# Kernel tuning notes

Hardware: AMD Instinct MI355X
Metric: run time of the kernel (lower is better)

## Reference

```python
import jax, jax.numpy as jnp
import numpy as np

N, F, R, E = 10000, 128, 20, 640000

def _linear_params(key, fan_in, fan_out):
    k1, k2 = jax.random.split(key)
    bound = 1.0 / np.sqrt(fan_in)
    W = jax.random.uniform(k1, (fan_in, fan_out), jnp.float32, -bound, bound)
    b = jax.random.uniform(k2, (fan_out,), jnp.float32, -bound, bound)
    return W, b

def _mlp(x, W1, b1, W2, b2):
    # Linear -> SiLU -> Linear on last axis
    return jax.nn.silu(x @ W1 + b1) @ W2 + b2


def setup_inputs() -> dict:
    key = jax.random.key(0)
    ks = jax.random.split(key, 12)
    s = jax.random.normal(ks[0], (N, F), jnp.float32)
    v = jax.random.normal(ks[1], (N, 3, F), jnp.float32)
    edge_index = jax.random.randint(ks[2], (2, E), 0, N, jnp.int32)
    rbf = jax.random.normal(ks[3], (E, R), jnp.float32)
    ms_w1, ms_b1 = _linear_params(ks[4], F + R, F)
    ms_w2, ms_b2 = _linear_params(ks[5], F, F)
    mv_w1, mv_b1 = _linear_params(ks[6], F + R, F)
    mv_w2, mv_b2 = _linear_params(ks[7], F, F)
    us_w1, us_b1 = _linear_params(ks[8], 2 * F, F)
    us_w2, us_b2 = _linear_params(ks[9], F, F)
    uv_w1, uv_b1 = _linear_params(ks[10], 2 * F, F)
    uv_w2, uv_b2 = _linear_params(ks[11], F, F)
    return dict(s=s, v=v, edge_index=edge_index, rbf=rbf,
                ms_w1=ms_w1, ms_b1=ms_b1, ms_w2=ms_w2, ms_b2=ms_b2,
                mv_w1=mv_w1, mv_b1=mv_b1, mv_w2=mv_w2, mv_b2=mv_b2,
                us_w1=us_w1, us_b1=us_b1, us_w2=us_w2, us_b2=us_b2,
                uv_w1=uv_w1, uv_b1=uv_b1, uv_w2=uv_w2, uv_b2=uv_b2)


def reference(s, v, edge_index, rbf,
              ms_w1, ms_b1, ms_w2, ms_b2,
              mv_w1, mv_b1, mv_w2, mv_b2,
              us_w1, us_b1, us_w2, us_b2,
              uv_w1, uv_b1, uv_w2, uv_b2):
    row, col = edge_index[0], edge_index[1]
    n_nodes = s.shape[0]
    s_row = s[row]                                  # [E, F]
    v_diff = v[row] - v[col]                        # [E, 3, F]
    s_msg = jnp.concatenate([s_row, rbf], axis=-1)  # [E, F+R]
    # per-edge vector message input: broadcast scalar features over the 3 axis
    v_msg = jnp.concatenate([
        jnp.broadcast_to(s_row[:, None, :], (s_row.shape[0], 3, s.shape[1])),
        jnp.broadcast_to(rbf[:, None, :], (rbf.shape[0], 3, rbf.shape[1])),
    ], axis=-1)                                     # [E, 3, F+R]
    ds = _mlp(s_msg, ms_w1, ms_b1, ms_w2, ms_b2)    # [E, F]
    dv = _mlp(v_msg, mv_w1, mv_b1, mv_w2, mv_b2)    # [E, 3, F]
    # normalize v_diff per (edge, feature) over the 3-vector axis
    v_norm = jnp.linalg.norm(v_diff, axis=1, keepdims=True)  # [E, 1, F]
    dv = dv * (v_diff / (v_norm + 1e-08))
    ds_agg = jax.ops.segment_sum(ds, col, num_segments=n_nodes)  # [N, F]
    dv_agg = jax.ops.segment_sum(dv, col, num_segments=n_nodes)  # [N, 3, F]
    s_out = s + _mlp(jnp.concatenate([s, ds_agg], axis=-1), us_w1, us_b1, us_w2, us_b2)
    v_out = v + _mlp(jnp.concatenate([v, dv_agg], axis=-1), uv_w1, uv_b1, uv_w2, uv_b2)
    return (s_out, v_out)
```

## Files before the change

### kernel.cpp

```cpp
#include <hip/hip_runtime.h>

#define FDIM 128
#define NEDGE 640000
#define NNODE 10000
#define K1PAD 160
#define HSTR 136

typedef __attribute__((ext_vector_type(8))) short short8;
typedef __attribute__((ext_vector_type(4))) float f32x4;
typedef __attribute__((ext_vector_type(4))) unsigned short ushort4_t;

static __device__ __forceinline__ unsigned short f2bf(float f){
  unsigned int u = __builtin_bit_cast(unsigned int, f);
  u += 0x7fffu + ((u >> 16) & 1u);
  return (unsigned short)(u >> 16);
}
static __device__ __forceinline__ short8 pack8(const float* x){
  short8 r;
#pragma unroll
  for (int i = 0; i < 8; ++i) r[i] = (short)f2bf(x[i]);
  return r;
}
static __device__ __forceinline__ short8 cvt8(float4 a, float4 b){
  float x[8] = {a.x, a.y, a.z, a.w, b.x, b.y, b.z, b.w};
  return pack8(x);
}
static __device__ __forceinline__ f32x4 mfma16(short8 a, short8 b, f32x4 c){
  return __builtin_amdgcn_mfma_f32_16x16x32_bf16(a, b, c, 0, 0, 0);
}
static __device__ __forceinline__ float silu(float p){
  return p * (1.f / (1.f + __expf(-p)));
}

__global__ __launch_bounds__(256) void prep_wt(
    const float* __restrict__ ms_w1, const float* __restrict__ mv_w1,
    const float* __restrict__ ms_w2, const float* __restrict__ mv_w2,
    const float* __restrict__ us_w1, const float* __restrict__ uv_w1,
    const float* __restrict__ us_w2, const float* __restrict__ uv_w2,
    unsigned short* __restrict__ wbuf)
{
  int i = blockIdx.x * 256 + threadIdx.x;
  if (i >= 172032) return;
  float val;
  if (i < 40960) {
    int t = (i < 20480) ? i : i - 20480;
    const float* src = (i < 20480) ? ms_w1 : mv_w1;
    int j = t / 160, k = t - j * 160;
    val = (k < 148) ? src[k * 128 + j] : 0.f;
  } else if (i < 73728) {
    int t = i - 40960;
    const float* src = (t < 16384) ? ms_w2 : mv_w2;
    t &= 16383;
    int j = t >> 7, k = t & 127;
    val = src[k * 128 + j];
  } else if (i < 139264) {
    int t = i - 73728;
    const float* src = (t < 32768) ? us_w1 : uv_w1;
    t &= 32767;
    int j = t >> 8, k = t & 255;
    val = src[k * 128 + j];
  } else {
    int t = i - 139264;
    const float* src = (t < 16384) ? us_w2 : uv_w2;
    t &= 16383;
    int j = t >> 7, k = t & 127;
    val = src[k * 128 + j];
  }
  wbuf[i] = f2bf(val);
}

__global__ __launch_bounds__(256) void prep_misc(
    const float* __restrict__ s, unsigned short* __restrict__ s_bf,
    float* __restrict__ zero_base)
{
  int i = blockIdx.x * 256 + threadIdx.x;
  if (i < 320000) {
    float4 p = *reinterpret_cast<const float4*>(s + i * 4);
    ushort4_t o;
    o[0] = f2bf(p.x); o[1] = f2bf(p.y); o[2] = f2bf(p.z); o[3] = f2bf(p.w);
    *reinterpret_cast<ushort4_t*>(s_bf + i * 4) = o;
  } else {
    int t = i - 320000;
    float4 z = {0.f, 0.f, 0.f, 0.f};
    *reinterpret_cast<float4*>(zero_base + t * 4) = z;
  }
}

__device__ __forceinline__ void run_mlp_edge(
    const short8 (&afrag)[2][5],
    const unsigned short* __restrict__ W1, const float* __restrict__ B1,
    const unsigned short* __restrict__ W2,
    unsigned short* hb, int g, int r16, f32x4 (&acc2)[2][8])
{
  f32x4 acc[2][8];
  const f32x4 z = {0.f, 0.f, 0.f, 0.f};
#pragma unroll
  for (int es = 0; es < 2; ++es)
#pragma unroll
    for (int nt = 0; nt < 8; ++nt) acc[es][nt] = z;
#pragma unroll
  for (int ks = 0; ks < 5; ++ks) {
#pragma unroll
    for (int nt = 0; nt < 8; ++nt) {
      const short8 w = *reinterpret_cast<const short8*>(W1 + (nt * 16 + r16) * K1PAD + ks * 32 + g * 8);
      acc[0][nt] = mfma16(afrag[0][ks], w, acc[0][nt]);
      acc[1][nt] = mfma16(afrag[1][ks], w, acc[1][nt]);
    }
  }
  float b1v[8];
#pragma unroll
  for (int nt = 0; nt < 8; ++nt) b1v[nt] = B1[nt * 16 + r16];
#pragma unroll
  for (int es = 0; es < 2; ++es)
#pragma unroll
    for (int nt = 0; nt < 8; ++nt)
#pragma unroll
      for (int r = 0; r < 4; ++r) {
        float p = acc[es][nt][r] + b1v[nt];
        hb[(es * 16 + g * 4 + r) * HSTR + nt * 16 + r16] = f2bf(silu(p));
      }
#pragma unroll
  for (int es = 0; es < 2; ++es)
#pragma unroll
    for (int nt = 0; nt < 8; ++nt) acc2[es][nt] = z;
#pragma unroll
  for (int ks = 0; ks < 4; ++ks) {
    const short8 a0 = *reinterpret_cast<const short8*>(hb + r16 * HSTR + ks * 32 + g * 8);
    const short8 a1 = *reinterpret_cast<const short8*>(hb + (16 + r16) * HSTR + ks * 32 + g * 8);
#pragma unroll
    for (int nt = 0; nt < 8; ++nt) {
      const short8 w = *reinterpret_cast<const short8*>(W2 + (nt * 16 + r16) * FDIM + ks * 32 + g * 8);
      acc2[0][nt] = mfma16(a0, w, acc2[0][nt]);
      acc2[1][nt] = mfma16(a1, w, acc2[1][nt]);
    }
  }
}

__global__ __launch_bounds__(256) void edge_kernel(
    const float* __restrict__ v,
    const int* __restrict__ erow, const int* __restrict__ ecol,
    const float* __restrict__ rbf,
    const unsigned short* __restrict__ s_bf,
    const unsigned short* __restrict__ wms1, const unsigned short* __restrict__ wms2,
    const float* __restrict__ ms_b1, const float* __restrict__ ms_b2,
    const unsigned short* __restrict__ wmv1, const unsigned short* __restrict__ wmv2,
    const float* __restrict__ mv_b1, const float* __restrict__ mv_b2,
    float* __restrict__ ds_agg, float* __restrict__ dv_agg)
{
  __shared__ unsigned short lds_h[4][32 * HSTR];
  const int tid = threadIdx.x;
  const int wid = tid >> 6, lane = tid & 63;
  const int g = lane >> 4, r16 = lane & 15;
  const int e0 = blockIdx.x * 128 + wid * 32;
  unsigned short* hb = &lds_h[wid][0];

  short8 afrag[2][5];
#pragma unroll
  for (int es = 0; es < 2; ++es) {
    const int e = e0 + es * 16 + r16;
    const int rA = erow[e];
    const unsigned short* sp = s_bf + rA * FDIM + g * 8;
#pragma unroll
    for (int ks = 0; ks < 4; ++ks)
      afrag[es][ks] = *reinterpret_cast<const short8*>(sp + ks * 32);
    float xr[8] = {0.f, 0.f, 0.f, 0.f, 0.f, 0.f, 0.f, 0.f};
    if (g < 2) {
      float4 p0 = *reinterpret_cast<const float4*>(rbf + e * 20 + g * 8);
      float4 p1 = *reinterpret_cast<const float4*>(rbf + e * 20 + g * 8 + 4);
      xr[0] = p0.x; xr[1] = p0.y; xr[2] = p0.z; xr[3] = p0.w;
      xr[4] = p1.x; xr[5] = p1.y; xr[6] = p1.z; xr[7] = p1.w;
    } else if (g == 2) {
      float4 p0 = *reinterpret_cast<const float4*>(rbf + e * 20 + 16);
      xr[0] = p0.x; xr[1] = p0.y; xr[2] = p0.z; xr[3] = p0.w;
    }
    afrag[es][4] = pack8(xr);
  }
  int dstE[2][4], rowE[2][4];
#pragma unroll
  for (int es = 0; es < 2; ++es)
#pragma unroll
    for (int r = 0; r < 4; ++r) {
      const int e = e0 + es * 16 + g * 4 + r;
      dstE[es][r] = ecol[e];
      rowE[es][r] = erow[e];
    }

  {
    f32x4 acc2[2][8];
    run_mlp_edge(afrag, wms1, ms_b1, wms2, hb, g, r16, acc2);
    float b2v[8];
#pragma unroll
    for (int nt = 0; nt < 8; ++nt) b2v[nt] = ms_b2[nt * 16 + r16];
#pragma unroll
    for (int es = 0; es < 2; ++es)
#pragma unroll
      for (int r = 0; r < 4; ++r) {
        float* dsa = ds_agg + dstE[es][r] * FDIM;
#pragma unroll
        for (int nt = 0; nt < 8; ++nt)
          unsafeAtomicAdd(dsa + nt * 16 + r16, acc2[es][nt][r] + b2v[nt]);
      }
  }
  {
    f32x4 acc2[2][8];
    run_mlp_edge(afrag, wmv1, mv_b1, wmv2, hb, g, r16, acc2);
    float b2v[8];
#pragma unroll
    for (int nt = 0; nt < 8; ++nt) b2v[nt] = mv_b2[nt * 16 + r16];
#pragma unroll
    for (int es = 0; es < 2; ++es)
#pragma unroll
      for (int r = 0; r < 4; ++r) {
        const float* vr = v + (long)rowE[es][r] * 384;
        const float* vc = v + (long)dstE[es][r] * 384;
        float* dva = dv_agg + dstE[es][r] * 384;
#pragma unroll
        for (int nt = 0; nt < 8; ++nt) {
          const int j = nt * 16 + r16;
          float d0 = vr[j] - vc[j];
          float d1 = vr[j + 128] - vc[j + 128];
          float d2 = vr[j + 256] - vc[j + 256];
          float nrm = sqrtf(d0 * d0 + d1 * d1 + d2 * d2);
          float base = (acc2[es][nt][r] + b2v[nt]) / (nrm + 1e-8f);
          unsafeAtomicAdd(dva + j, base * d0);
          unsafeAtomicAdd(dva + j + 128, base * d1);
          unsafeAtomicAdd(dva + j + 256, base * d2);
        }
      }
  }
}

__global__ __launch_bounds__(256) void node_kernel(
    const float* __restrict__ xin,
    const float* __restrict__ agg,
    const unsigned short* __restrict__ W1T,
    const float* __restrict__ b1,
    const unsigned short* __restrict__ W2T,
    const float* __restrict__ b2,
    float* __restrict__ outp,
    int nrows)
{
  __shared__ unsigned short lds_h[4][32 * HSTR];
  const int tid = threadIdx.x;
  const int wid = tid >> 6, lane = tid & 63;
  const int g = lane >> 4, r16 = lane & 15;
  const int n0 = blockIdx.x * 128 + wid * 32;
  unsigned short* hb = &lds_h[wid][0];

  short8 afrag[2][8];
#pragma unroll
  for (int es = 0; es < 2; ++es) {
    int n = n0 + es * 16 + r16;
    if (n >= nrows) n = nrows - 1;
    const float* xp = xin + (long)n * FDIM + g * 8;
    const float* ap = agg + (long)n * FDIM + g * 8;
#pragma unroll
    for (int ks = 0; ks < 4; ++ks) {
      float4 p0 = *reinterpret_cast<const float4*>(xp + ks * 32);
      float4 p1 = *reinterpret_cast<const float4*>(xp + ks * 32 + 4);
      afrag[es][ks] = cvt8(p0, p1);
    }
#pragma unroll
    for (int ks = 0; ks < 4; ++ks) {
      float4 p0 = *reinterpret_cast<const float4*>(ap + ks * 32);
      float4 p1 = *reinterpret_cast<const float4*>(ap + ks * 32 + 4);
      afrag[es][4 + ks] = cvt8(p0, p1);
    }
  }
  f32x4 acc[2][8];
  const f32x4 z = {0.f, 0.f, 0.f, 0.f};
#pragma unroll
  for (int es = 0; es < 2; ++es)
#pragma unroll
    for (int nt = 0; nt < 8; ++nt) acc[es][nt] = z;
#pragma unroll
  for (int ks = 0; ks < 8; ++ks) {
#pragma unroll
    for (int nt = 0; nt < 8; ++nt) {
      const short8 w = *reinterpret_cast<const short8*>(W1T + (nt * 16 + r16) * 256 + ks * 32 + g * 8);
      acc[0][nt] = mfma16(afrag[0][ks], w, acc[0][nt]);
      acc[1][nt] = mfma16(afrag[1][ks], w, acc[1][nt]);
    }
  }
  float b1v[8];
#pragma unroll
  for (int nt = 0; nt < 8; ++nt) b1v[nt] = b1[nt * 16 + r16];
#pragma unroll
  for (int es = 0; es < 2; ++es)
#pragma unroll
    for (int nt = 0; nt < 8; ++nt)
#pragma unroll
      for (int r = 0; r < 4; ++r) {
        float p = acc[es][nt][r] + b1v[nt];
        hb[(es * 16 + g * 4 + r) * HSTR + nt * 16 + r16] = f2bf(silu(p));
      }
  f32x4 acc2[2][8];
#pragma unroll
  for (int es = 0; es < 2; ++es)
#pragma unroll
    for (int nt = 0; nt < 8; ++nt) acc2[es][nt] = z;
#pragma unroll
  for (int ks = 0; ks < 4; ++ks) {
    const short8 a0 = *reinterpret_cast<const short8*>(hb + r16 * HSTR + ks * 32 + g * 8);
    const short8 a1 = *reinterpret_cast<const short8*>(hb + (16 + r16) * HSTR + ks * 32 + g * 8);
#pragma unroll
    for (int nt = 0; nt < 8; ++nt) {
      const short8 w = *reinterpret_cast<const short8*>(W2T + (nt * 16 + r16) * FDIM + ks * 32 + g * 8);
      acc2[0][nt] = mfma16(a0, w, acc2[0][nt]);
      acc2[1][nt] = mfma16(a1, w, acc2[1][nt]);
    }
  }
  float b2v[8];
#pragma unroll
  for (int nt = 0; nt < 8; ++nt) b2v[nt] = b2[nt * 16 + r16];
#pragma unroll
  for (int es = 0; es < 2; ++es)
#pragma unroll
    for (int r = 0; r < 4; ++r) {
      const int n = n0 + es * 16 + g * 4 + r;
      if (n < nrows) {
#pragma unroll
        for (int nt = 0; nt < 8; ++nt) {
          const int j = nt * 16 + r16;
          outp[(long)n * FDIM + j] = xin[(long)n * FDIM + j] + acc2[es][nt][r] + b2v[nt];
        }
      }
    }
}

extern "C" void kernel_launch(void* const* d_in, const int* in_sizes, int n_in,
                              void* d_out, int out_size, void* d_ws, size_t ws_size,
                              hipStream_t stream) {
  const float* s     = (const float*)d_in[0];
  const float* v     = (const float*)d_in[1];
  const int*   eidx  = (const int*)d_in[2];
  const float* rbf   = (const float*)d_in[3];
  const float* ms_w1 = (const float*)d_in[4];  const float* ms_b1 = (const float*)d_in[5];
  const float* ms_w2 = (const float*)d_in[6];  const float* ms_b2 = (const float*)d_in[7];
  const float* mv_w1 = (const float*)d_in[8];  const float* mv_b1 = (const float*)d_in[9];
  const float* mv_w2 = (const float*)d_in[10]; const float* mv_b2 = (const float*)d_in[11];
  const float* us_w1 = (const float*)d_in[12]; const float* us_b1 = (const float*)d_in[13];
  const float* us_w2 = (const float*)d_in[14]; const float* us_b2 = (const float*)d_in[15];
  const float* uv_w1 = (const float*)d_in[16]; const float* uv_b1 = (const float*)d_in[17];
  const float* uv_w2 = (const float*)d_in[18]; const float* uv_b2 = (const float*)d_in[19];

  char* ws = (char*)d_ws;
  float* ds_agg = (float*)(ws);
  float* dv_agg = (float*)(ws + 5120000);
  unsigned short* s_bf = (unsigned short*)(ws + 20480000);
  unsigned short* wbuf = (unsigned short*)(ws + 23040000);

  prep_wt<<<672, 256, 0, stream>>>(ms_w1, mv_w1, ms_w2, mv_w2,
                                   us_w1, uv_w1, us_w2, uv_w2, wbuf);
  prep_misc<<<6250, 256, 0, stream>>>(s, s_bf, ds_agg);

  edge_kernel<<<5000, 256, 0, stream>>>(
      v, eidx, eidx + NEDGE, rbf, s_bf,
      wbuf + 0,      wbuf + 40960,  ms_b1, ms_b2,
      wbuf + 20480,  wbuf + 57344,  mv_b1, mv_b2,
      ds_agg, dv_agg);

  float* outp = (float*)d_out;
  node_kernel<<<79, 256, 0, stream>>>(s, ds_agg, wbuf + 73728, us_b1,
                                      wbuf + 139264, us_b2, outp, NNODE);
  node_kernel<<<235, 256, 0, stream>>>(v, dv_agg, wbuf + 106496, uv_b1,
                                       wbuf + 155648, uv_b2, outp + NNODE * FDIM, 3 * NNODE);
}
```

Baseline: 1.646 ms.

## Sort edges by destination into CSR and aggregate per node without atomics

Adds histogram, scan and scatter kernels that build a destination-sorted edge permutation (CSR). The edge MLP kernel becomes one wavefront per destination node: it walks that node's incoming edges in chunks of 32 and sums ds and dv in registers, then reduces across lanes and writes each node's result once. This removes the per-edge float atomics into ds_agg and dv_agg, and the separate zeroing of those buffers. In exchange it adds preprocessing launches, including a single-block scan, wasted padded lanes on partial chunks, and load imbalance when node degrees differ.

```diff
diff --git a/kernel.cpp b/kernel.cpp
--- a/kernel.cpp
+++ b/kernel.cpp
@@ -69,9 +69,8 @@
   wbuf[i] = f2bf(val);
 }
 
-__global__ __launch_bounds__(256) void prep_misc(
-    const float* __restrict__ s, unsigned short* __restrict__ s_bf,
-    float* __restrict__ zero_base)
+__global__ __launch_bounds__(256) void prep_s(
+    const float* __restrict__ s, unsigned short* __restrict__ s_bf)
 {
   int i = blockIdx.x * 256 + threadIdx.x;
   if (i < 320000) {
@@ -79,17 +78,60 @@
     ushort4_t o;
     o[0] = f2bf(p.x); o[1] = f2bf(p.y); o[2] = f2bf(p.z); o[3] = f2bf(p.w);
     *reinterpret_cast<ushort4_t*>(s_bf + i * 4) = o;
-  } else {
-    int t = i - 320000;
-    float4 z = {0.f, 0.f, 0.f, 0.f};
-    *reinterpret_cast<float4*>(zero_base + t * 4) = z;
+  }
+}
+
+__global__ __launch_bounds__(256) void hist_kernel(
+    const int* __restrict__ ecol, int* __restrict__ deg)
+{
+  int e = blockIdx.x * 256 + threadIdx.x;
+  if (e < NEDGE) atomicAdd(&deg[ecol[e]], 1);
+}
+
+__global__ __launch_bounds__(256) void scan_kernel(
+    const int* __restrict__ deg, int* __restrict__ offs)
+{
+  __shared__ int part[256];
+  const int t = threadIdx.x;
+  const int base = t * 40;
+  int sum = 0;
+  for (int i = 0; i < 40; ++i) {
+    int idx = base + i;
+    if (idx < NNODE) sum += deg[idx];
+  }
+  part[t] = sum;
+  __syncthreads();
+  for (int off = 1; off < 256; off <<= 1) {
+    int vv = (t >= off) ? part[t - off] : 0;
+    __syncthreads();
+    if (t >= off) part[t] += vv;
+    __syncthreads();
+  }
+  int run = (t == 0) ? 0 : part[t - 1];
+  for (int i = 0; i < 40; ++i) {
+    int idx = base + i;
+    if (idx < NNODE) { offs[idx] = run; run += deg[idx]; }
+  }
+  if (t == 255) offs[NNODE] = run;
+}
+
+__global__ __launch_bounds__(256) void scatter_kernel(
+    const int* __restrict__ ecol, const int* __restrict__ offs,
+    int* __restrict__ cnt, int* __restrict__ eperm)
+{
+  int e = blockIdx.x * 256 + threadIdx.x;
+  if (e < NEDGE) {
+    int n = ecol[e];
+    int p = atomicAdd(&cnt[n], 1);
+    eperm[offs[n] + p] = e;
   }
 }
 
 __device__ __forceinline__ void run_mlp_edge(
     const short8 (&afrag)[2][5],
-    const unsigned short* __restrict__ W1, const float* __restrict__ B1,
+    const unsigned short* __restrict__ W1,
     const unsigned short* __restrict__ W2,
+    const float* __restrict__ B1,
     unsigned short* hb, int g, int r16, f32x4 (&acc2)[2][8])
 {
   f32x4 acc[2][8];
@@ -136,97 +178,126 @@
   }
 }
 
-__global__ __launch_bounds__(256) void edge_kernel(
+__global__ __launch_bounds__(64) void edge_agg_kernel(
     const float* __restrict__ v,
-    const int* __restrict__ erow, const int* __restrict__ ecol,
-    const float* __restrict__ rbf,
+    const int* __restrict__ erow, const float* __restrict__ rbf,
     const unsigned short* __restrict__ s_bf,
     const unsigned short* __restrict__ wms1, const unsigned short* __restrict__ wms2,
     const float* __restrict__ ms_b1, const float* __restrict__ ms_b2,
     const unsigned short* __restrict__ wmv1, const unsigned short* __restrict__ wmv2,
     const float* __restrict__ mv_b1, const float* __restrict__ mv_b2,
+    const int* __restrict__ offs, const int* __restrict__ eperm,
     float* __restrict__ ds_agg, float* __restrict__ dv_agg)
 {
-  __shared__ unsigned short lds_h[4][32 * HSTR];
-  const int tid = threadIdx.x;
-  const int wid = tid >> 6, lane = tid & 63;
+  __shared__ unsigned short hb[32 * HSTR];
+  const int n = blockIdx.x;
+  const int lane = threadIdx.x;
   const int g = lane >> 4, r16 = lane & 15;
-  const int e0 = blockIdx.x * 128 + wid * 32;
-  unsigned short* hb = &lds_h[wid][0];
-
-  short8 afrag[2][5];
-#pragma unroll
-  for (int es = 0; es < 2; ++es) {
-    const int e = e0 + es * 16 + r16;
-    const int rA = erow[e];
-    const unsigned short* sp = s_bf + rA * FDIM + g * 8;
-#pragma unroll
-    for (int ks = 0; ks < 4; ++ks)
-      afrag[es][ks] = *reinterpret_cast<const short8*>(sp + ks * 32);
-    float xr[8] = {0.f, 0.f, 0.f, 0.f, 0.f, 0.f, 0.f, 0.f};
-    if (g < 2) {
-      float4 p0 = *reinterpret_cast<const float4*>(rbf + e * 20 + g * 8);
-      float4 p1 = *reinterpret_cast<const float4*>(rbf + e * 20 + g * 8 + 4);
-      xr[0] = p0.x; xr[1] = p0.y; xr[2] = p0.z; xr[3] = p0.w;
-      xr[4] = p1.x; xr[5] = p1.y; xr[6] = p1.z; xr[7] = p1.w;
-    } else if (g == 2) {
-      float4 p0 = *reinterpret_cast<const float4*>(rbf + e * 20 + 16);
-      xr[0] = p0.x; xr[1] = p0.y; xr[2] = p0.z; xr[3] = p0.w;
-    }
-    afrag[es][4] = pack8(xr);
-  }
-  int dstE[2][4], rowE[2][4];
-#pragma unroll
-  for (int es = 0; es < 2; ++es)
-#pragma unroll
-    for (int r = 0; r < 4; ++r) {
-      const int e = e0 + es * 16 + g * 4 + r;
-      dstE[es][r] = ecol[e];
-      rowE[es][r] = erow[e];
-    }
-
-  {
-    f32x4 acc2[2][8];
-    run_mlp_edge(afrag, wms1, ms_b1, wms2, hb, g, r16, acc2);
-    float b2v[8];
-#pragma unroll
-    for (int nt = 0; nt < 8; ++nt) b2v[nt] = ms_b2[nt * 16 + r16];
+  const int beg = offs[n], end = offs[n + 1];
+  const int deg = end - beg;
+
+  float dsT[8];
+  float dvT0[8], dvT1[8], dvT2[8];
+#pragma unroll
+  for (int nt = 0; nt < 8; ++nt) { dsT[nt] = 0.f; dvT0[nt] = 0.f; dvT1[nt] = 0.f; dvT2[nt] = 0.f; }
+
+  const float* vcn = v + (long)n * 384;
+
+  for (int t0 = 0; t0 < deg; t0 += 32) {
+    short8 afrag[2][5];
+#pragma unroll
+    for (int es = 0; es < 2; ++es) {
+      int sidx = t0 + es * 16 + r16;
+      if (sidx >= deg) sidx = deg - 1;
+      const int e = eperm[beg + sidx];
+      const unsigned short* sp = s_bf + (long)erow[e] * FDIM + g * 8;
+#pragma unroll
+      for (int ks = 0; ks < 4; ++ks)
+        afrag[es][ks] = *reinterpret_cast<const short8*>(sp + ks * 32);
+      float xr[8] = {0.f, 0.f, 0.f, 0.f, 0.f, 0.f, 0.f, 0.f};
+      if (g < 2) {
+        float4 p0 = *reinterpret_cast<const float4*>(rbf + (long)e * 20 + g * 8);
+        float4 p1 = *reinterpret_cast<const float4*>(rbf + (long)e * 20 + g * 8 + 4);
+        xr[0] = p0.x; xr[1] = p0.y; xr[2] = p0.z; xr[3] = p0.w;
+        xr[4] = p1.x; xr[5] = p1.y; xr[6] = p1.z; xr[7] = p1.w;
+      } else if (g == 2) {
+        float4 p0 = *reinterpret_cast<const float4*>(rbf + (long)e * 20 + 16);
+        xr[0] = p0.x; xr[1] = p0.y; xr[2] = p0.z; xr[3] = p0.w;
+      }
+      afrag[es][4] = pack8(xr);
+    }
+    int rowE[2][4];
+    bool okE[2][4];
 #pragma unroll
     for (int es = 0; es < 2; ++es)
 #pragma unroll
       for (int r = 0; r < 4; ++r) {
-        float* dsa = ds_agg + dstE[es][r] * FDIM;
-#pragma unroll
-        for (int nt = 0; nt < 8; ++nt)
-          unsafeAtomicAdd(dsa + nt * 16 + r16, acc2[es][nt][r] + b2v[nt]);
+        int sidx = t0 + es * 16 + g * 4 + r;
+        okE[es][r] = (sidx < deg);
+        if (sidx >= deg) sidx = deg - 1;
+        rowE[es][r] = erow[eperm[beg + sidx]];
       }
-  }
-  {
-    f32x4 acc2[2][8];
-    run_mlp_edge(afrag, wmv1, mv_b1, wmv2, hb, g, r16, acc2);
-    float b2v[8];
-#pragma unroll
-    for (int nt = 0; nt < 8; ++nt) b2v[nt] = mv_b2[nt * 16 + r16];
-#pragma unroll
-    for (int es = 0; es < 2; ++es)
-#pragma unroll
-      for (int r = 0; r < 4; ++r) {
-        const float* vr = v + (long)rowE[es][r] * 384;
-        const float* vc = v + (long)dstE[es][r] * 384;
-        float* dva = dv_agg + dstE[es][r] * 384;
-#pragma unroll
-        for (int nt = 0; nt < 8; ++nt) {
-          const int j = nt * 16 + r16;
-          float d0 = vr[j] - vc[j];
-          float d1 = vr[j + 128] - vc[j + 128];
-          float d2 = vr[j + 256] - vc[j + 256];
-          float nrm = sqrtf(d0 * d0 + d1 * d1 + d2 * d2);
-          float base = (acc2[es][nt][r] + b2v[nt]) / (nrm + 1e-8f);
-          unsafeAtomicAdd(dva + j, base * d0);
-          unsafeAtomicAdd(dva + j + 128, base * d1);
-          unsafeAtomicAdd(dva + j + 256, base * d2);
+
+    {
+      f32x4 acc2[2][8];
+      run_mlp_edge(afrag, wms1, wms2, ms_b1, hb, g, r16, acc2);
+#pragma unroll
+      for (int es = 0; es < 2; ++es)
+#pragma unroll
+        for (int r = 0; r < 4; ++r)
+#pragma unroll
+          for (int nt = 0; nt < 8; ++nt)
+            dsT[nt] += okE[es][r] ? acc2[es][nt][r] : 0.f;
+    }
+    {
+      f32x4 acc2[2][8];
+      run_mlp_edge(afrag, wmv1, wmv2, mv_b1, hb, g, r16, acc2);
+      float b2v[8];
+#pragma unroll
+      for (int nt = 0; nt < 8; ++nt) b2v[nt] = mv_b2[nt * 16 + r16];
+#pragma unroll
+      for (int es = 0; es < 2; ++es)
+#pragma unroll
+        for (int r = 0; r < 4; ++r) {
+          const float* vr = v + (long)rowE[es][r] * 384;
+          const bool ok = okE[es][r];
+#pragma unroll
+          for (int nt = 0; nt < 8; ++nt) {
+            const int j = nt * 16 + r16;
+            float d0 = vr[j]       - vcn[j];
+            float d1 = vr[j + 128] - vcn[j + 128];
+            float d2 = vr[j + 256] - vcn[j + 256];
+            float nrm = sqrtf(d0 * d0 + d1 * d1 + d2 * d2);
+            float base = (acc2[es][nt][r] + b2v[nt]) / (nrm + 1e-8f);
+            if (ok) {
+              dvT0[nt] += base * d0;
+              dvT1[nt] += base * d1;
+              dvT2[nt] += base * d2;
+            }
+          }
         }
-      }
+    }
+  }
+
+#pragma unroll
+  for (int nt = 0; nt < 8; ++nt) {
+    dsT[nt]  += __shfl_xor(dsT[nt], 16);  dsT[nt]  += __shfl_xor(dsT[nt], 32);
+    dvT0[nt] += __shfl_xor(dvT0[nt], 16); dvT0[nt] += __shfl_xor(dvT0[nt], 32);
+    dvT1[nt] += __shfl_xor(dvT1[nt], 16); dvT1[nt] += __shfl_xor(dvT1[nt], 32);
+    dvT2[nt] += __shfl_xor(dvT2[nt], 16); dvT2[nt] += __shfl_xor(dvT2[nt], 32);
+  }
+
+  if (g == 0) {
+    const float fdeg = (float)deg;
+#pragma unroll
+    for (int nt = 0; nt < 8; ++nt)
+      ds_agg[(long)n * FDIM + nt * 16 + r16] = dsT[nt] + fdeg * ms_b2[nt * 16 + r16];
+  } else {
+#pragma unroll
+    for (int nt = 0; nt < 8; ++nt) {
+      float val = (g == 1) ? dvT0[nt] : (g == 2) ? dvT1[nt] : dvT2[nt];
+      dv_agg[(long)n * 384 + (g - 1) * 128 + nt * 16 + r16] = val;
+    }
   }
 }
 
@@ -349,16 +420,27 @@
   float* dv_agg = (float*)(ws + 5120000);
   unsigned short* s_bf = (unsigned short*)(ws + 20480000);
   unsigned short* wbuf = (unsigned short*)(ws + 23040000);
+  int* deg   = (int*)(ws + 23384064);
+  int* cnt   = (int*)(ws + 23424064);
+  int* offs  = (int*)(ws + 23464064);
+  int* eperm = (int*)(ws + 23504068);
+
+  const int* ecol = eidx + NEDGE;
+
+  hipMemsetAsync(deg, 0, 80000, stream);
 
   prep_wt<<<672, 256, 0, stream>>>(ms_w1, mv_w1, ms_w2, mv_w2,
                                    us_w1, uv_w1, us_w2, uv_w2, wbuf);
-  prep_misc<<<6250, 256, 0, stream>>>(s, s_bf, ds_agg);
-
-  edge_kernel<<<5000, 256, 0, stream>>>(
-      v, eidx, eidx + NEDGE, rbf, s_bf,
-      wbuf + 0,      wbuf + 40960,  ms_b1, ms_b2,
-      wbuf + 20480,  wbuf + 57344,  mv_b1, mv_b2,
-      ds_agg, dv_agg);
+  prep_s<<<1250, 256, 0, stream>>>(s, s_bf);
+  hist_kernel<<<2500, 256, 0, stream>>>(ecol, deg);
+  scan_kernel<<<1, 256, 0, stream>>>(deg, offs);
+  scatter_kernel<<<2500, 256, 0, stream>>>(ecol, offs, cnt, eperm);
+
+  edge_agg_kernel<<<NNODE, 64, 0, stream>>>(
+      v, eidx, rbf, s_bf,
+      wbuf + 0,     wbuf + 40960, ms_b1, ms_b2,
+      wbuf + 20480, wbuf + 57344, mv_b1, mv_b2,
+      offs, eperm, ds_agg, dv_agg);
 
   float* outp = (float*)d_out;
   node_kernel<<<79, 256, 0, stream>>>(s, ds_agg, wbuf + 73728, us_b1,
```

Measured after the change: 2.116 ms. +28.5%, slower.
